# Performance work log

Measured on AMD Instinct MI355X. Metric: run time of the kernel, lower is better.

Reference implementation:

```python
import jax, jax.numpy as jnp
import numpy as np
import math

INPUT_DIM, HIDDEN, OUT_DIM, NUM_LAYERS = 128, 512, 128, 2
GRID_SIZE, ORDER = 5, 3  # efficient-KAN defaults
NBASIS = GRID_SIZE + ORDER  # 8 basis functions per input feature


def _grid():
    h = 2.0 / GRID_SIZE  # grid_range [-1, 1]
    return jnp.asarray(np.arange(-ORDER, GRID_SIZE + ORDER + 1) * h - 1.0, dtype=jnp.float32)  # [12]


def b_splines(x, grid):
    # x: [B, In] -> [B, In, NBASIS] via Cox-de Boor recursion (order 3)
    x = x[..., None]
    bases = ((x >= grid[:-1]) & (x < grid[1:])).astype(x.dtype)
    for p in range(1, ORDER + 1):
        left = (x - grid[:-(p + 1)]) / (grid[p:-1] - grid[:-(p + 1)]) * bases[..., :-1]
        right = (grid[p + 1:] - x) / (grid[p + 1:] - grid[1:-p]) * bases[..., 1:]
        bases = left + right
    return bases


def kan_layer(x, base_w, spline_w, grid):
    # efficient-KAN: silu base branch + B-spline branch
    B = x.shape[0]
    out = jax.nn.silu(x) @ base_w.T
    spl = b_splines(x, grid).reshape(B, -1) @ spline_w.reshape(spline_w.shape[0], -1).T
    return out + spl


def lstm_cell(inp, h, c, w_ih, w_hh, b_ih, b_hh, kan_base, kan_spline, grid):
    gates = inp @ w_ih.T + b_ih + h @ w_hh.T + b_hh  # [B, 3H]
    i_g, f_g, o_g = jnp.split(jax.nn.sigmoid(gates), 3, axis=1)
    g = kan_layer(jnp.concatenate([inp, h], axis=1), kan_base, kan_spline, grid)
    c_next = f_g * c + i_g * g
    h_next = o_g * jnp.tanh(c_next)
    return h_next, c_next


def setup_inputs() -> dict:
    key = jax.random.key(0)
    ks = jax.random.split(key, 32)
    stdv = 1.0 / math.sqrt(HIDDEN)
    u = lambda k, shape: jax.random.uniform(k, shape, jnp.float32, -stdv, stdv)
    d = {"x": jax.random.normal(ks[0], (64, 256, INPUT_DIM), jnp.float32)}
    for L in range(NUM_LAYERS):
        In = INPUT_DIM if L == 0 else HIDDEN
        b = 8 * L
        d[f"w_ih{L}"] = u(ks[b + 1], (3 * HIDDEN, In))
        d[f"w_hh{L}"] = u(ks[b + 2], (3 * HIDDEN, HIDDEN))
        d[f"b_ih{L}"] = jnp.zeros((3 * HIDDEN,), jnp.float32)
        d[f"b_hh{L}"] = jnp.zeros((3 * HIDDEN,), jnp.float32)
        d[f"kan_base{L}"] = u(ks[b + 3], (HIDDEN, In + HIDDEN))
        d[f"kan_spline{L}"] = u(ks[b + 4], (HIDDEN, In + HIDDEN, NBASIS)) * 0.1
    d["fc_w"] = u(ks[20], (OUT_DIM, HIDDEN))
    d["fc_b"] = u(ks[21], (OUT_DIM,))
    return d


def reference(x, w_ih0, w_hh0, b_ih0, b_hh0, kan_base0, kan_spline0,
              w_ih1, w_hh1, b_ih1, b_hh1, kan_base1, kan_spline1, fc_w, fc_b):
    grid = _grid()
    B = x.shape[0]
    layers = [
        (w_ih0, w_hh0, b_ih0, b_hh0, kan_base0, kan_spline0),
        (w_ih1, w_hh1, b_ih1, b_hh1, kan_base1, kan_spline1),
    ]
    h0 = tuple(jnp.zeros((B, HIDDEN), x.dtype) for _ in range(NUM_LAYERS))
    c0 = tuple(jnp.zeros((B, HIDDEN), x.dtype) for _ in range(NUM_LAYERS))

    def step(carry, x_t):
        hs, cs = carry
        hs, cs = list(hs), list(cs)
        inp = x_t
        for L in range(NUM_LAYERS):
            w_ih, w_hh, b_ih, b_hh, kb, ksw = layers[L]
            hs[L], cs[L] = lstm_cell(inp, hs[L], cs[L], w_ih, w_hh, b_ih, b_hh, kb, ksw, grid)
            inp = hs[L]
        return (tuple(hs), tuple(cs)), None

    xs = jnp.swapaxes(x, 0, 1)  # [T, B, D]
    (hs, _), _ = jax.lax.scan(step, (h0, c0), xs)
    return hs[-1] @ fc_w.T + fc_b
```

## Files before the change

kernel.cpp:

```cpp
#include <hip/hip_runtime.h>
#include <math.h>
#include <stdint.h>

namespace {

typedef __attribute__((ext_vector_type(8))) short short8v;
typedef __attribute__((ext_vector_type(4))) float f32x4;

constexpr int TT = 256;

constexpr size_t OFF_ST = 0;
constexpr size_t OFF_P0 = 98304;
constexpr size_t OFF_P1 = 884736;
constexpr size_t OFF_WF = 1671168;
constexpr size_t OFF_FF = 11894784;
constexpr size_t WS_NEED = 12959744ull * 4;

constexpr size_t WFLO = 10223616;
constexpr size_t FFLO = 1064960;
constexpr size_t FLB1 = 409600;

__device__ __forceinline__ float sigmoidf_(float v) { return 1.0f / (1.0f + expf(-v)); }

__device__ __forceinline__ ushort bf16h(float v) {
    uint32_t u = __float_as_uint(v);
    return (ushort)((u + 0x7fffu + ((u >> 16) & 1u)) >> 16);
}
__device__ __forceinline__ float bf16f(ushort h) { return __uint_as_float(((uint32_t)h) << 16); }

__device__ __forceinline__ void bspline8(float x, float* out) {
    const float KG[12] = {-2.2f,-1.8f,-1.4f,-1.0f,-0.6f,-0.2f,
                           0.2f, 0.6f, 1.0f, 1.4f, 1.8f, 2.2f};
    float b[11];
#pragma unroll
    for (int i = 0; i < 11; ++i)
        b[i] = (x >= KG[i] && x < KG[i + 1]) ? 1.0f : 0.0f;
#pragma unroll
    for (int p = 1; p <= 3; ++p) {
#pragma unroll
        for (int i = 0; i + p < 11; ++i) {
            float l = (x - KG[i])         * (1.0f / (KG[i + p] - KG[i]));
            float r = (KG[i + p + 1] - x) * (1.0f / (KG[i + p + 1] - KG[i + 1]));
            b[i] = l * b[i] + r * b[i + 1];
        }
    }
#pragma unroll
    for (int i = 0; i < 8; ++i) out[i] = b[i];
}

__device__ __forceinline__ void putFeat(int l, int k, int b, float z,
                                        ushort* __restrict__ fe)
{
    const int NSL = l ? 16 : 10, KC = l ? 512 : 320;
    const int kh = (k >= KC) ? 1 : 0, kr = k - kh * KC;
    const int sl = kr >> 5, kg = (kr >> 3) & 3, j = kr & 7;
    const size_t cell = (size_t)((b >> 4) * 64 + (b & 15) + 16 * kg) * 8 + j;
    const size_t LB = l ? FLB1 : 0;
    const size_t slb = ((size_t)kh * NSL + sl) * 2048 + cell;
    const size_t pstep = (size_t)2 * NSL * 2048;

    auto putp = [&](int p, float v) {
        size_t idx = LB + (size_t)p * pstep + slb;
        ushort h = bf16h(v);
        fe[idx] = h;
        fe[FFLO + idx] = bf16h(v - bf16f(h));
    };
    putp(0, z);
    putp(1, z / (1.0f + expf(-z)));
    float bs[8];
    bspline8(z, bs);
#pragma unroll
    for (int r = 0; r < 8; ++r) putp(2 + r, bs[r]);
}

__global__ __launch_bounds__(256) void sentinel_kernel(float* out, float v) {
    int i = blockIdx.x * 256 + threadIdx.x;
    if (i < 8192) out[i] = v;
}

__global__ __launch_bounds__(256) void wbuild_kernel(
    ushort* __restrict__ wf,
    const float* __restrict__ w_ih0, const float* __restrict__ w_hh0,
    const float* __restrict__ kb0, const float* __restrict__ ksp0,
    const float* __restrict__ w_ih1, const float* __restrict__ w_hh1,
    const float* __restrict__ kb1, const float* __restrict__ ksp1)
{
    const int gid = blockIdx.x * 256 + threadIdx.x;
    const int s = gid >> 6, lane = gid & 63;
    int wid, sl;
    if (s < 7680) { wid = s / 10; sl = s % 10; }
    else          { wid = 768 + (s - 7680) / 16; sl = (s - 7680) % 16; }
    const int l = wid >= 768 ? 1 : 0;
    const int r2 = wid - l * 768;
    const int kh = r2 >= 384 ? 1 : 0;
    const int tile = r2 - kh * 384;
    const int IN = l ? 512 : 128, W = IN + 512, KC = W >> 1;
    const int m = lane & 15, kg = lane >> 4;
    const int k0 = kh * KC + sl * 32;
    const int kk = k0 + kg * 8;
    const int o0 = tile * 16;

    const float* w_ih = l ? w_ih1 : w_ih0;
    const float* w_hh = l ? w_hh1 : w_hh0;
    const float* kb   = l ? kb1 : kb0;
    const float* ksp  = l ? ksp1 : ksp0;

    float vv[8];
    if (tile < 96) {
        const int row = o0 + m;
#pragma unroll
        for (int j = 0; j < 8; ++j) {
            const int k = kk + j;
            vv[j] = (k0 < IN) ? w_ih[(size_t)row * IN + k]
                              : w_hh[(size_t)row * 512 + (k - IN)];
        }
    } else if (tile < 128) {
        const int row = (tile - 96) * 16 + m;
#pragma unroll
        for (int j = 0; j < 8; ++j) vv[j] = kb[(size_t)row * W + kk + j];
    } else {
        const int rr = (tile - 128) >> 5, op = ((tile - 128) & 31) * 16 + m;
#pragma unroll
        for (int j = 0; j < 8; ++j)
            vv[j] = ksp[((size_t)op * W + kk + j) * 8 + rr];
    }
    const size_t base = (size_t)s * 512 + (size_t)lane * 8;
#pragma unroll
    for (int j = 0; j < 8; ++j) {
        ushort h = bf16h(vv[j]);
        wf[base + j] = h;
        wf[WFLO + base + j] = bf16h(vv[j] - bf16f(h));
    }
}

__global__ __launch_bounds__(256) void prologue_kernel(
    const float* __restrict__ x, float* __restrict__ ws)
{
    ushort* fe = (ushort*)(ws + OFF_FF);
    const int g = blockIdx.x * 256 + threadIdx.x;
    if (g < 98304) {
        ws[OFF_ST + g] = 0.0f;
    } else if (g < 106496) {
        const int i = g - 98304, k = i & 127, b = i >> 7;
        putFeat(0, k, b, x[((size_t)b * TT) * 128 + k], fe);
    } else if (g < 139264) {
        const int i = g - 106496, o = i & 511, b = i >> 9;
        putFeat(0, 128 + o, b, 0.0f, fe);
    } else {
        const int i = g - 139264, o = i & 511, b = i >> 9;
        putFeat(1, 512 + o, b, 0.0f, fe);
    }
}

__global__ __launch_bounds__(256) void phaseA_kernel(
    float* __restrict__ ws, int s)
{
    __shared__ short8v sfh[2][256], sfl[2][256];

    const int t = threadIdx.x, lane = t & 63;
    const int wv = __builtin_amdgcn_readfirstlane(t >> 6);
    const int bid = blockIdx.x;
    const int l  = bid >= 192 ? 1 : 0;
    if (l ? (s < 1) : (s >= TT)) return;
    const int r3 = bid - l * 192;
    const int kh = r3 >= 96 ? 1 : 0;
    const int grp = r3 - kh * 96;
    const int tile = grp * 4 + wv;
    const int NSL = l ? 16 : 10;
    const int p = (grp < 24) ? 0 : (grp < 32) ? 1 : (2 + ((grp - 32) >> 3));

    const ushort* wf = (const ushort*)(ws + OFF_WF);
    const ushort* fe = (const ushort*)(ws + OFF_FF);
    float* pout = ws + (l ? OFF_P1 : OFF_P0) + (size_t)kh * 393216;

    const int wid = l * 768 + kh * 384 + tile;
    const size_t sbase = l ? (7680 + (size_t)(wid - 768) * 16) : (size_t)wid * 10;
    const size_t fbase = (l ? FLB1 : 0) +
                         ((size_t)(p * 2 + kh) * NSL) * 2048;

    const int m = lane & 15, kg = lane >> 4;
    const int o0 = tile * 16;

    f32x4 acc[4] = {{0,0,0,0},{0,0,0,0},{0,0,0,0},{0,0,0,0}};

    {
        short8v rh = *(const short8v*)(fe + fbase + (size_t)t * 8);
        short8v rl = *(const short8v*)(fe + FFLO + fbase + (size_t)t * 8);
        sfh[0][t] = rh; sfl[0][t] = rl;
    }
    short8v cwh = *(const short8v*)(wf + sbase * 512 + (size_t)lane * 8);
    short8v cwl = *(const short8v*)(wf + WFLO + sbase * 512 + (size_t)lane * 8);
    __syncthreads();

    int cur = 0;
    for (int sl = 0; sl < NSL; ++sl) {
        const bool hasNext = (sl + 1 < NSL);
        short8v nfh, nfl, nwh, nwl;
        if (hasNext) {
            const size_t nb = fbase + (size_t)(sl + 1) * 2048 + (size_t)t * 8;
            nfh = *(const short8v*)(fe + nb);
            nfl = *(const short8v*)(fe + FFLO + nb);
            const size_t wb = (sbase + sl + 1) * 512 + (size_t)lane * 8;
            nwh = *(const short8v*)(wf + wb);
            nwl = *(const short8v*)(wf + WFLO + wb);
        }

#pragma unroll
        for (int bt = 0; bt < 4; ++bt) {
            short8v bh = sfh[cur][bt * 64 + lane];
            short8v bl = sfl[cur][bt * 64 + lane];
            acc[bt] = __builtin_amdgcn_mfma_f32_16x16x32_bf16(cwh, bh, acc[bt], 0, 0, 0);
            acc[bt] = __builtin_amdgcn_mfma_f32_16x16x32_bf16(cwh, bl, acc[bt], 0, 0, 0);
            acc[bt] = __builtin_amdgcn_mfma_f32_16x16x32_bf16(cwl, bh, acc[bt], 0, 0, 0);
        }

        if (hasNext) {
            sfh[cur ^ 1][t] = nfh;
            sfl[cur ^ 1][t] = nfl;
            cwh = nwh; cwl = nwl;
            __syncthreads();
            cur ^= 1;
        }
    }

#pragma unroll
    for (int bt = 0; bt < 4; ++bt) {
        float* dst = pout + (size_t)(bt * 16 + m) * 6144 + o0 + kg * 4;
        *(float4*)dst = (float4){acc[bt][0], acc[bt][1], acc[bt][2], acc[bt][3]};
    }
}

__global__ __launch_bounds__(256) void phaseB_kernel(
    float* __restrict__ ws,
    const float* __restrict__ b_ih0, const float* __restrict__ b_hh0,
    const float* __restrict__ b_ih1, const float* __restrict__ b_hh1,
    const float* __restrict__ x, int s)
{
    ushort* fe = (ushort*)(ws + OFF_FF);
    float* c0T = ws + OFF_ST;
    float* h1T = c0T + 32768;
    float* c1T = h1T + 32768;
    const float* p0 = ws + OFF_P0;
    const float* p1 = ws + OFF_P1;

    const int u = blockIdx.x * 256 + threadIdx.x;
    if (u < 32768) {
        if (s >= TT) return;
        const int o = u & 511, b = u >> 9;
        auto P = [&](int rw) {
            return p0[(size_t)b * 6144 + rw] + p0[393216 + (size_t)b * 6144 + rw];
        };
        float si = P(o)        + b_ih0[o]        + b_hh0[o];
        float sf = P(512 + o)  + b_ih0[512 + o]  + b_hh0[512 + o];
        float sO = P(1024 + o) + b_ih0[1024 + o] + b_hh0[1024 + o];
        float sk = P(1536 + o);
#pragma unroll
        for (int rr = 0; rr < 8; ++rr) sk += P(2048 + rr * 512 + o);
        float ig = sigmoidf_(si), fg = sigmoidf_(sf), og = sigmoidf_(sO);
        float c = fg * c0T[(size_t)b * 512 + o] + ig * sk;
        c0T[(size_t)b * 512 + o] = c;
        float z = og * tanhf(c);
        putFeat(1, o, b, z, fe);
        putFeat(0, 128 + o, b, z, fe);
    } else if (u < 65536) {
        if (s < 1) return;
        const int v = u - 32768, o = v & 511, b = v >> 9;
        auto P = [&](int rw) {
            return p1[(size_t)b * 6144 + rw] + p1[393216 + (size_t)b * 6144 + rw];
        };
        float si = P(o)        + b_ih1[o]        + b_hh1[o];
        float sf = P(512 + o)  + b_ih1[512 + o]  + b_hh1[512 + o];
        float sO = P(1024 + o) + b_ih1[1024 + o] + b_hh1[1024 + o];
        float sk = P(1536 + o);
#pragma unroll
        for (int rr = 0; rr < 8; ++rr) sk += P(2048 + rr * 512 + o);
        float ig = sigmoidf_(si), fg = sigmoidf_(sf), og = sigmoidf_(sO);
        float c = fg * c1T[(size_t)b * 512 + o] + ig * sk;
        c1T[(size_t)b * 512 + o] = c;
        float z = og * tanhf(c);
        h1T[(size_t)b * 512 + o] = z;
        putFeat(1, 512 + o, b, z, fe);
    } else {
        if (s + 1 >= TT) return;
        const int v = u - 65536, k = v & 127, b = v >> 7;
        putFeat(0, k, b, x[((size_t)b * TT + (s + 1)) * 128 + k], fe);
    }
}

__global__ __launch_bounds__(256) void final_fc(
    const float* __restrict__ h1T, const float* __restrict__ fc_w,
    const float* __restrict__ fc_b, float* __restrict__ out)
{
    const int gid = blockIdx.x * 256 + threadIdx.x;
    const int b = gid & 63, jo = gid >> 6;
    float a = fc_b[jo];
    const float* hr = h1T + (size_t)b * 512;
    const float* wr = fc_w + (size_t)jo * 512;
    for (int o = 0; o < 512; o += 4) {
        float4 h4 = *(const float4*)(hr + o);
        float4 w4 = *(const float4*)(wr + o);
        a = fmaf(h4.x, w4.x, a); a = fmaf(h4.y, w4.y, a);
        a = fmaf(h4.z, w4.z, a); a = fmaf(h4.w, w4.w, a);
    }
    out[(size_t)b * 128 + jo] = a;
}

}

extern "C" void kernel_launch(void* const* d_in, const int* in_sizes, int n_in,
                              void* d_out, int out_size, void* d_ws, size_t ws_size,
                              hipStream_t stream) {
    (void)out_size;
    float* out = (float*)d_out;

    static const int EXP_SIZES[15] = {
        64 * 256 * 128, 1536 * 128, 1536 * 512, 1536, 1536,
        512 * 640, 512 * 640 * 8,
        1536 * 512, 1536 * 512, 1536, 1536,
        512 * 1024, 512 * 1024 * 8,
        128 * 512, 128
    };
    if (n_in != 15) { sentinel_kernel<<<32, 256, 0, stream>>>(out, 111.0f); return; }
    for (int i = 0; i < 15; ++i)
        if (in_sizes[i] != EXP_SIZES[i]) {
            sentinel_kernel<<<32, 256, 0, stream>>>(out, 200.0f * (i + 1)); return;
        }
    if (ws_size < WS_NEED) { sentinel_kernel<<<32, 256, 0, stream>>>(out, 7777.0f); return; }

    const float* x     = (const float*)d_in[0];
    const float* w_ih0 = (const float*)d_in[1];
    const float* w_hh0 = (const float*)d_in[2];
    const float* b_ih0 = (const float*)d_in[3];
    const float* b_hh0 = (const float*)d_in[4];
    const float* kb0   = (const float*)d_in[5];
    const float* ksp0  = (const float*)d_in[6];
    const float* w_ih1 = (const float*)d_in[7];
    const float* w_hh1 = (const float*)d_in[8];
    const float* b_ih1 = (const float*)d_in[9];
    const float* b_hh1 = (const float*)d_in[10];
    const float* kb1   = (const float*)d_in[11];
    const float* ksp1  = (const float*)d_in[12];
    const float* fc_w  = (const float*)d_in[13];
    const float* fc_b  = (const float*)d_in[14];

    float* ws = (float*)d_ws;

    prologue_kernel<<<672, 256, 0, stream>>>(x, ws);
    wbuild_kernel<<<4992, 256, 0, stream>>>((ushort*)(ws + OFF_WF),
        w_ih0, w_hh0, kb0, ksp0, w_ih1, w_hh1, kb1, ksp1);

    for (int s = 0; s <= TT; ++s) {
        phaseA_kernel<<<384, 256, 0, stream>>>(ws, s);
        phaseB_kernel<<<288, 256, 0, stream>>>(
            ws, b_ih0, b_hh0, b_ih1, b_hh1, x, s);
    }

    final_fc<<<32, 256, 0, stream>>>(ws + OFF_ST + 32768, fc_w, fc_b, out);
}
```

Baseline: 5.670 ms.

## Split phaseA into 2-wave blocks with XCD-interleaved task mapping; resize phaseB grid

PhaseA now launches 768 blocks of 128 threads instead of 384 blocks of 256. Each thread stages two feature vectors into shared memory so the tile layout is unchanged. Block IDs are remapped (bid&7 selects a group of tasks) so neighbouring tiles are spread across the chiplets. PhaseB runs 256 blocks, one per CU, and each block handles 288 items, with 32 threads doing a second item. The intent is better load balance and less time per step in the latency-bound recurrent loop, at the cost of more blocks each sharing fewer waves per barrier.

```diff
diff --git a/kernel.cpp b/kernel.cpp
--- a/kernel.cpp
+++ b/kernel.cpp
@@ -152,22 +152,24 @@
     }
 }
 
-__global__ __launch_bounds__(256) void phaseA_kernel(
+__global__ __launch_bounds__(128) void phaseA_kernel(
     float* __restrict__ ws, int s)
 {
     __shared__ short8v sfh[2][256], sfl[2][256];
 
-    const int t = threadIdx.x, lane = t & 63;
+    const int t = threadIdx.x;
+    const int lane = t & 63;
     const int wv = __builtin_amdgcn_readfirstlane(t >> 6);
     const int bid = blockIdx.x;
-    const int l  = bid >= 192 ? 1 : 0;
+    const int task = ((bid & 7) * 96) + (bid >> 3);
+    const int l  = task >= 384 ? 1 : 0;
     if (l ? (s < 1) : (s >= TT)) return;
-    const int r3 = bid - l * 192;
-    const int kh = r3 >= 96 ? 1 : 0;
-    const int grp = r3 - kh * 96;
-    const int tile = grp * 4 + wv;
+    const int r3 = task - l * 384;
+    const int kh = r3 >= 192 ? 1 : 0;
+    const int g2 = r3 - kh * 192;
+    const int tile = g2 * 2 + wv;
     const int NSL = l ? 16 : 10;
-    const int p = (grp < 24) ? 0 : (grp < 32) ? 1 : (2 + ((grp - 32) >> 3));
+    const int p = (g2 < 48) ? 0 : (g2 < 64) ? 1 : (2 + ((g2 - 64) >> 4));
 
     const ushort* wf = (const ushort*)(ws + OFF_WF);
     const ushort* fe = (const ushort*)(ws + OFF_FF);
@@ -184,9 +186,11 @@
     f32x4 acc[4] = {{0,0,0,0},{0,0,0,0},{0,0,0,0},{0,0,0,0}};
 
     {
-        short8v rh = *(const short8v*)(fe + fbase + (size_t)t * 8);
-        short8v rl = *(const short8v*)(fe + FFLO + fbase + (size_t)t * 8);
-        sfh[0][t] = rh; sfl[0][t] = rl;
+        const size_t b0 = fbase + (size_t)t * 8;
+        sfh[0][t]       = *(const short8v*)(fe + b0);
+        sfl[0][t]       = *(const short8v*)(fe + FFLO + b0);
+        sfh[0][t + 128] = *(const short8v*)(fe + b0 + 1024);
+        sfl[0][t + 128] = *(const short8v*)(fe + FFLO + b0 + 1024);
     }
     short8v cwh = *(const short8v*)(wf + sbase * 512 + (size_t)lane * 8);
     short8v cwl = *(const short8v*)(wf + WFLO + sbase * 512 + (size_t)lane * 8);
@@ -195,11 +199,13 @@
     int cur = 0;
     for (int sl = 0; sl < NSL; ++sl) {
         const bool hasNext = (sl + 1 < NSL);
-        short8v nfh, nfl, nwh, nwl;
+        short8v nf0h, nf0l, nf1h, nf1l, nwh, nwl;
         if (hasNext) {
             const size_t nb = fbase + (size_t)(sl + 1) * 2048 + (size_t)t * 8;
-            nfh = *(const short8v*)(fe + nb);
-            nfl = *(const short8v*)(fe + FFLO + nb);
+            nf0h = *(const short8v*)(fe + nb);
+            nf0l = *(const short8v*)(fe + FFLO + nb);
+            nf1h = *(const short8v*)(fe + nb + 1024);
+            nf1l = *(const short8v*)(fe + FFLO + nb + 1024);
             const size_t wb = (sbase + sl + 1) * 512 + (size_t)lane * 8;
             nwh = *(const short8v*)(wf + wb);
             nwl = *(const short8v*)(wf + WFLO + wb);
@@ -215,8 +221,10 @@
         }
 
         if (hasNext) {
-            sfh[cur ^ 1][t] = nfh;
-            sfl[cur ^ 1][t] = nfl;
+            sfh[cur ^ 1][t]       = nf0h;
+            sfl[cur ^ 1][t]       = nf0l;
+            sfh[cur ^ 1][t + 128] = nf1h;
+            sfl[cur ^ 1][t + 128] = nf1l;
             cwh = nwh; cwl = nwl;
             __syncthreads();
             cur ^= 1;
@@ -230,8 +238,8 @@
     }
 }
 
-__global__ __launch_bounds__(256) void phaseB_kernel(
-    float* __restrict__ ws,
+__device__ __forceinline__ void phaseB_item(
+    int u, float* __restrict__ ws,
     const float* __restrict__ b_ih0, const float* __restrict__ b_hh0,
     const float* __restrict__ b_ih1, const float* __restrict__ b_hh1,
     const float* __restrict__ x, int s)
@@ -243,7 +251,6 @@
     const float* p0 = ws + OFF_P0;
     const float* p1 = ws + OFF_P1;
 
-    const int u = blockIdx.x * 256 + threadIdx.x;
     if (u < 32768) {
         if (s >= TT) return;
         const int o = u & 511, b = u >> 9;
@@ -287,6 +294,18 @@
     }
 }
 
+__global__ __launch_bounds__(256) void phaseB_kernel(
+    float* __restrict__ ws,
+    const float* __restrict__ b_ih0, const float* __restrict__ b_hh0,
+    const float* __restrict__ b_ih1, const float* __restrict__ b_hh1,
+    const float* __restrict__ x, int s)
+{
+    const int base = blockIdx.x * 288;
+    phaseB_item(base + threadIdx.x, ws, b_ih0, b_hh0, b_ih1, b_hh1, x, s);
+    if (threadIdx.x < 32)
+        phaseB_item(base + 256 + threadIdx.x, ws, b_ih0, b_hh0, b_ih1, b_hh1, x, s);
+}
+
 __global__ __launch_bounds__(256) void final_fc(
     const float* __restrict__ h1T, const float* __restrict__ fc_w,
     const float* __restrict__ fc_b, float* __restrict__ out)
@@ -350,8 +369,8 @@
         w_ih0, w_hh0, kb0, ksp0, w_ih1, w_hh1, kb1, ksp1);
 
     for (int s = 0; s <= TT; ++s) {
-        phaseA_kernel<<<384, 256, 0, stream>>>(ws, s);
-        phaseB_kernel<<<288, 256, 0, stream>>>(
+        phaseA_kernel<<<768, 128, 0, stream>>>(ws, s);
+        phaseB_kernel<<<256, 256, 0, stream>>>(
             ws, b_ih0, b_hh0, b_ih1, b_hh1, x, s);
     }
 
```

After: 5.523 ms. 1.03x faster.
